# Optimization experiments

Hardware: AMD Instinct MI355X
Metric: run time of the kernel (lower is better)

## Reference

```python
import jax, jax.numpy as jnp
import numpy as np

N = 8192      # nodes
E = 16384     # edges
G = 512       # graphs
IN = 235      # node feature dim (input_dim)
H = 64        # hidden_dim
ED = 52       # edge feature dim


def setup_inputs() -> dict:
    key = jax.random.key(0)
    ks = jax.random.split(key, 24)
    s = lambda fan_in: 1.0 / np.sqrt(fan_in)
    inp = {}
    inp["x"] = jax.random.normal(ks[0], (N, IN), dtype=jnp.float32)
    inp["edge_index"] = jax.random.randint(ks[1], (2, E), 0, N)
    inp["edge_attr"] = jax.random.uniform(ks[2], (E, ED), dtype=jnp.float32)
    inp["batch"] = jnp.sort(jax.random.randint(ks[3], (N,), 0, G))
    # EdgeModel (nn of nnconv1): Linear(52,128) -> Linear(128, 235*64)
    inp["W1"] = jax.random.normal(ks[4], (128, ED), dtype=jnp.float32) * s(ED)
    inp["b1"] = jnp.zeros((128,), jnp.float32)
    inp["W2"] = jax.random.normal(ks[5], (IN * H, 128), dtype=jnp.float32) * s(128)
    inp["b2"] = jnp.zeros((IN * H,), jnp.float32)
    # NNConv root weight and bias
    inp["root"] = jax.random.normal(ks[6], (IN, H), dtype=jnp.float32) * s(IN)
    inp["conv_b"] = jnp.zeros((H,), jnp.float32)
    # MLP head
    inp["fw1"] = jax.random.normal(ks[7], (128, H), dtype=jnp.float32) * s(H)
    inp["fb1"] = jnp.zeros((128,), jnp.float32)
    inp["fw2"] = jax.random.normal(ks[8], (256, 128), dtype=jnp.float32) * s(128)
    inp["fb2"] = jnp.zeros((256,), jnp.float32)
    inp["fw3"] = jax.random.normal(ks[9], (128, 256), dtype=jnp.float32) * s(256)
    inp["fb3"] = jnp.zeros((128,), jnp.float32)
    inp["fw4"] = jax.random.normal(ks[10], (1, 128), dtype=jnp.float32) * s(128)
    inp["fb4"] = jnp.zeros((1,), jnp.float32)
    return inp


def reference(x, edge_index, edge_attr, batch, W1, b1, W2, b2, root, conv_b,
              fw1, fb1, fw2, fb2, fw3, fb3, fw4, fb4):
    src, dst = edge_index[0], edge_index[1]
    # edge MLP -> per-edge weight matrices [E, IN, H]
    h = edge_attr @ W1.T + b1
    w = (h @ W2.T + b2).reshape(E, IN, H)
    # gather source node feats, per-edge matmul, scatter-add to destinations
    msg = jnp.einsum('ei,eih->eh', x[src], w)          # [E, H]
    agg = jax.ops.segment_sum(msg, dst, num_segments=N)  # [N, H]
    out = jax.nn.relu(agg + x @ root + conv_b)           # NNConv + ReLU
    # global mean pool per graph
    summ = jax.ops.segment_sum(out, batch, num_segments=G)
    cnt = jax.ops.segment_sum(jnp.ones((N, 1), out.dtype), batch, num_segments=G)
    pooled = summ / jnp.maximum(cnt, 1.0)                # [G, H]
    # dense MLP head
    y = jax.nn.relu(pooled @ fw1.T + fb1)
    y = jax.nn.relu(y @ fw2.T + fb2)
    y = jax.nn.relu(y @ fw3.T + fb3)
    return y @ fw4.T + fb4                               # [G, 1]
```

## Files before the change

### kernel.cpp

```cpp
#include <hip/hip_runtime.h>
#include <hip/hip_bf16.h>
#include <stdint.h>

#define N_NODES 8192
#define N_EDGES 16384
#define N_GRAPHS 512
#define IN_DIM 235
#define H_DIM 64
#define ED_DIM 52
#define HID1 128
#define KP 256
#define NB 3328
#define NBE 3456

typedef __bf16 bf16x8 __attribute__((ext_vector_type(8)));
typedef float f32x4 __attribute__((ext_vector_type(4)));

static __device__ inline unsigned short f2bf(float f) {
    union { float f; unsigned u; } v; v.f = f;
    unsigned r = v.u + 0x7FFFu + ((v.u >> 16) & 1u);
    return (unsigned short)(r >> 16);
}
static __device__ inline float bf2f(unsigned short s) {
    union { unsigned u; float f; } v; v.u = ((unsigned)s) << 16;
    return v.f;
}

__global__ __launch_bounds__(256) void k_build_bt(const float* __restrict__ W1,
                                                  const float* __restrict__ W2,
                                                  unsigned short* __restrict__ Bt) {
    __shared__ float w1s[13 * HID1];
    __shared__ float w2s[64 * 132];
    const int i = blockIdx.x;
    const int by = blockIdx.y;
    const int t = threadIdx.x;
    const int dbase = by * 13;
    for (int j = t; j < 13 * HID1; j += 256) {
        const int dd = j >> 7, k = j & 127;
        w1s[j] = W1[k * ED_DIM + dbase + dd];
    }
    const float* w2src = W2 + (size_t)i * 64 * HID1;
    for (int j = t; j < 64 * HID1; j += 256) w2s[(j >> 7) * 132 + (j & 127)] = w2src[j];
    __syncthreads();
    const int pend = by * 832 + 832;
    for (int p = by * 832 + t; p < pend; p += 256) {
        const int dd = (p >> 6) - dbase, h = p & 63;
        const float4* w1v = (const float4*)&w1s[dd * HID1];
        const float4* w2v = (const float4*)&w2s[h * 132];
        float acc = 0.f;
        #pragma unroll
        for (int k4 = 0; k4 < HID1 / 4; ++k4) {
            const float4 a = w1v[k4], b = w2v[k4];
            acc += a.x * b.x + a.y * b.y + a.z * b.z + a.w * b.w;
        }
        Bt[(size_t)p * KP + i] = f2bf(acc);
    }
}

__global__ __launch_bounds__(256) void k_build_bc(const float* __restrict__ W2,
                                                  const float* __restrict__ b1,
                                                  const float* __restrict__ b2,
                                                  float* __restrict__ bc) {
    const int j = blockIdx.x * 256 + threadIdx.x;
    if (j >= IN_DIM * H_DIM) return;
    float acc = b2[j];
    const float* w = W2 + (size_t)j * HID1;
    #pragma unroll 8
    for (int k = 0; k < HID1; ++k) acc += w[k] * b1[k];
    bc[j] = acc;
}

__global__ __launch_bounds__(256) void k_build_ext(const float* __restrict__ root,
                                                   const float* __restrict__ bc,
                                                   unsigned short* __restrict__ Bt) {
    const int j = blockIdx.x;
    const int i = threadIdx.x;
    if (i >= IN_DIM) return;
    const float v = (j < 64) ? root[i * H_DIM + j] : bc[i * H_DIM + (j - 64)];
    Bt[(size_t)(NB + j) * KP + i] = f2bf(v);
}

__global__ __launch_bounds__(256) void k_build_a(const float* __restrict__ x,
                                                 unsigned short* __restrict__ A) {
    const int j = blockIdx.x * 256 + threadIdx.x;
    const int n = j >> 8, i = j & 255;
    A[j] = (i < IN_DIM) ? f2bf(x[n * IN_DIM + i]) : (unsigned short)0;
}

__global__ __launch_bounds__(256) void k_gemm(const unsigned short* __restrict__ A,
                                              const unsigned short* __restrict__ Bt,
                                              unsigned short* __restrict__ P,
                                              float* __restrict__ agg,
                                              float* __restrict__ xb2,
                                              const float* __restrict__ conv_b) {
    __shared__ unsigned short As[2 * 128 * 32];
    __shared__ unsigned short Bs[2 * 128 * 32];
    const int t = threadIdx.x;
    const int m0 = blockIdx.y * 128, n0 = blockIdx.x * 128;
    const int wid = t >> 6, lane = t & 63;
    const int wm = wid >> 1, wn = wid & 1;
    const int q = lane >> 4, r16 = lane & 15;

    f32x4 acc[4][4] = {};

    auto stage = [&](int k0, int buf) {
        #pragma unroll
        for (int r = 0; r < 2; ++r) {
            const int idx = r * 256 + t;
            const int row = idx >> 2;
            const int lgrp = ((idx & 3) ^ ((row >> 1) & 3)) * 8;
            const unsigned short* ga = &A[(size_t)(m0 + row) * KP + k0 + lgrp];
            const unsigned short* gb = &Bt[(size_t)(n0 + row) * KP + k0 + lgrp];
            char* la = (char*)As + buf * 8192 + r * 4096 + wid * 1024;
            char* lb = (char*)Bs + buf * 8192 + r * 4096 + wid * 1024;
            __builtin_amdgcn_global_load_lds(
                (const __attribute__((address_space(1))) unsigned int*)ga,
                (__attribute__((address_space(3))) unsigned int*)la, 16, 0, 0);
            __builtin_amdgcn_global_load_lds(
                (const __attribute__((address_space(1))) unsigned int*)gb,
                (__attribute__((address_space(3))) unsigned int*)lb, 16, 0, 0);
        }
    };

    stage(0, 0);
    const int pcq = (q ^ ((r16 >> 1) & 3)) * 8;
    #pragma unroll
    for (int it = 0; it < 8; ++it) {
        __syncthreads();
        if (it < 7) stage((it + 1) * 32, (it + 1) & 1);
        const int bo = (it & 1) * 4096;
        bf16x8 af[4], bfr[4];
        #pragma unroll
        for (int mi = 0; mi < 4; ++mi)
            af[mi] = *(const bf16x8*)(&As[bo + (wm * 64 + mi * 16 + r16) * 32 + pcq]);
        #pragma unroll
        for (int ni = 0; ni < 4; ++ni)
            bfr[ni] = *(const bf16x8*)(&Bs[bo + (wn * 64 + ni * 16 + r16) * 32 + pcq]);
        #pragma unroll
        for (int mi = 0; mi < 4; ++mi)
            #pragma unroll
            for (int ni = 0; ni < 4; ++ni)
                acc[mi][ni] = __builtin_amdgcn_mfma_f32_16x16x32_bf16(
                    bfr[ni], af[mi], acc[mi][ni], 0, 0, 0);
    }

    if (n0 < NB) {
        #pragma unroll
        for (int mi = 0; mi < 4; ++mi)
            #pragma unroll
            for (int ni = 0; ni < 4; ++ni) {
                const int row = m0 + wm * 64 + mi * 16 + r16;
                const int col = n0 + wn * 64 + ni * 16 + q * 4;
                union { unsigned short us[4]; uint2 u2; } pk;
                #pragma unroll
                for (int rr = 0; rr < 4; ++rr) pk.us[rr] = f2bf(acc[mi][ni][rr]);
                *(uint2*)(&P[(size_t)row * NB + col]) = pk.u2;
            }
    } else {
        #pragma unroll
        for (int mi = 0; mi < 4; ++mi)
            #pragma unroll
            for (int ni = 0; ni < 4; ++ni) {
                const int row = m0 + wm * 64 + mi * 16 + r16;
                const int cl = ni * 16 + q * 4;
                if (wn == 0) {
                    const float4 cb = *(const float4*)&conv_b[cl];
                    float4 v;
                    v.x = acc[mi][ni][0] + cb.x; v.y = acc[mi][ni][1] + cb.y;
                    v.z = acc[mi][ni][2] + cb.z; v.w = acc[mi][ni][3] + cb.w;
                    *(float4*)(&agg[row * H_DIM + cl]) = v;
                } else {
                    float4 v;
                    v.x = acc[mi][ni][0]; v.y = acc[mi][ni][1];
                    v.z = acc[mi][ni][2]; v.w = acc[mi][ni][3];
                    *(float4*)(&xb2[row * H_DIM + cl]) = v;
                }
            }
    }
}

__global__ __launch_bounds__(256) void k_edge(const int* __restrict__ ei,
                                              const float* __restrict__ ea,
                                              const unsigned short* __restrict__ P,
                                              const float* __restrict__ xb2,
                                              float* __restrict__ agg) {
    const int e = (blockIdx.x * 256 + threadIdx.x) >> 6;
    const int h = threadIdx.x & 63;
    if (e >= N_EDGES) return;
    const int s = ei[e], dst = ei[N_EDGES + e];
    const unsigned short* Pr = P + (size_t)s * NB + h;
    const float* ear = ea + (size_t)e * ED_DIM;

    float eav[ED_DIM];
    #pragma unroll
    for (int d4 = 0; d4 < ED_DIM / 4; ++d4)
        *(float4*)&eav[d4 * 4] = *(const float4*)&ear[d4 * 4];

    unsigned short pv[ED_DIM];
    #pragma unroll
    for (int d = 0; d < ED_DIM; ++d) pv[d] = Pr[d * H_DIM];

    float acc = xb2[s * H_DIM + h];
    #pragma unroll
    for (int d = 0; d < ED_DIM; ++d) acc += eav[d] * bf2f(pv[d]);
    atomicAdd(&agg[dst * H_DIM + h], acc);
}

__global__ __launch_bounds__(256) void k_pool(const float* __restrict__ agg,
                                              const int* __restrict__ batch,
                                              float* __restrict__ psum,
                                              float* __restrict__ pcnt) {
    const int n = (blockIdx.x * 256 + threadIdx.x) >> 6;
    const int h = threadIdx.x & 63;
    if (n >= N_NODES) return;
    const float v = fmaxf(agg[n * H_DIM + h], 0.f);
    const int g = batch[n];
    atomicAdd(&psum[g * H_DIM + h], v);
    if (h == 0) atomicAdd(&pcnt[g], 1.0f);
}

__global__ __launch_bounds__(256) void k_head(const float* __restrict__ psum,
                                              const float* __restrict__ pcnt,
                                              const float* __restrict__ fw1, const float* __restrict__ fb1,
                                              const float* __restrict__ fw2, const float* __restrict__ fb2,
                                              const float* __restrict__ fw3, const float* __restrict__ fb3,
                                              const float* __restrict__ fw4, const float* __restrict__ fb4,
                                              float* __restrict__ out) {
    __shared__ float sp[64], s1[128], s2[256], s3[128];
    const int g = blockIdx.x, t = threadIdx.x;
    if (t < 64) sp[t] = psum[g * 64 + t] / fmaxf(pcnt[g], 1.0f);
    __syncthreads();
    if (t < 128) {
        float a = fb1[t];
        const float* w = fw1 + t * 64;
        #pragma unroll 8
        for (int k = 0; k < 64; ++k) a += sp[k] * w[k];
        s1[t] = fmaxf(a, 0.f);
    }
    __syncthreads();
    {
        float a = fb2[t];
        const float* w = fw2 + t * 128;
        #pragma unroll 8
        for (int k = 0; k < 128; ++k) a += s1[k] * w[k];
        s2[t] = fmaxf(a, 0.f);
    }
    __syncthreads();
    if (t < 128) {
        float a = fb3[t];
        const float* w = fw3 + t * 256;
        #pragma unroll 8
        for (int k = 0; k < 256; ++k) a += s2[k] * w[k];
        s3[t] = fmaxf(a, 0.f);
    }
    __syncthreads();
    if (t < 64) {
        float p = s3[t] * fw4[t] + s3[t + 64] * fw4[t + 64];
        #pragma unroll
        for (int off = 32; off > 0; off >>= 1) p += __shfl_down(p, off);
        if (t == 0) out[g] = p + fb4[0];
    }
}

extern "C" void kernel_launch(void* const* d_in, const int* in_sizes, int n_in,
                              void* d_out, int out_size, void* d_ws, size_t ws_size,
                              hipStream_t stream) {
    const float* x      = (const float*)d_in[0];
    const int*   ei     = (const int*)d_in[1];
    const float* ea     = (const float*)d_in[2];
    const int*   batch  = (const int*)d_in[3];
    const float* W1     = (const float*)d_in[4];
    const float* b1     = (const float*)d_in[5];
    const float* W2     = (const float*)d_in[6];
    const float* b2     = (const float*)d_in[7];
    const float* root   = (const float*)d_in[8];
    const float* conv_b = (const float*)d_in[9];
    const float* fw1 = (const float*)d_in[10]; const float* fb1 = (const float*)d_in[11];
    const float* fw2 = (const float*)d_in[12]; const float* fb2 = (const float*)d_in[13];
    const float* fw3 = (const float*)d_in[14]; const float* fb3 = (const float*)d_in[15];
    const float* fw4 = (const float*)d_in[16]; const float* fb4 = (const float*)d_in[17];
    float* out = (float*)d_out;

    char* ws = (char*)d_ws;
    unsigned short* A   = (unsigned short*)(ws);
    unsigned short* Bt  = (unsigned short*)(ws + 4194304);
    unsigned short* P   = (unsigned short*)(ws + 5963776);
    float* agg  = (float*)(ws + 60489728);
    float* xb2  = (float*)(ws + 62586880);
    float* bc   = (float*)(ws + 64684032);
    float* psum = (float*)(ws + 64744192);
    float* pcnt = (float*)(ws + 64875264);

    hipMemsetAsync(Bt, 0, (size_t)NBE * KP * sizeof(unsigned short), stream);
    hipMemsetAsync(psum, 0, (size_t)(N_GRAPHS * H_DIM + N_GRAPHS) * sizeof(float), stream);

    k_build_bc<<<dim3((IN_DIM * H_DIM + 255) / 256), dim3(256), 0, stream>>>(W2, b1, b2, bc);
    k_build_bt<<<dim3(IN_DIM, 4), dim3(256), 0, stream>>>(W1, W2, Bt);
    k_build_ext<<<dim3(128), dim3(256), 0, stream>>>(root, bc, Bt);
    k_build_a<<<dim3(N_NODES), dim3(256), 0, stream>>>(x, A);
    k_gemm<<<dim3(NBE / 128, N_NODES / 128), dim3(256), 0, stream>>>(A, Bt, P, agg, xb2, conv_b);
    k_edge<<<dim3(N_EDGES / 4), dim3(256), 0, stream>>>(ei, ea, P, xb2, agg);
    k_pool<<<dim3(N_NODES / 4), dim3(256), 0, stream>>>(agg, batch, psum, pcnt);
    k_head<<<dim3(N_GRAPHS), dim3(256), 0, stream>>>(psum, pcnt, fw1, fb1, fw2, fb2, fw3, fb3, fw4, fb4, out);
}
```

Measured before the change: 228.8 us.

## Enlarge GEMM tile to 256x256 with 8 waves and fuse bias build into ext

The GEMM goes from 128x128 tiles with 4 waves to 256x256 tiles with 8 waves. Each wave now computes 128x64 (8x4 MFMA tiles), so every loaded fragment is reused more and the kernel does less global-to-LDS traffic. The B matrix is padded from 3456 to 3584 rows to fit the larger tile, and the extra padded columns are skipped in the epilogue. The separate bias-combination kernel is folded into k_build_ext, removing one launch. The cost is more accumulator registers, fewer blocks on the grid, and some wasted work on the padded columns.

```diff
diff --git a/kernel.cpp b/kernel.cpp
--- a/kernel.cpp
+++ b/kernel.cpp
@@ -12,6 +12,7 @@
 #define KP 256
 #define NB 3328
 #define NBE 3456
+#define NBP 3584
 
 typedef __bf16 bf16x8 __attribute__((ext_vector_type(8)));
 typedef float f32x4 __attribute__((ext_vector_type(4)));
@@ -57,26 +58,25 @@
     }
 }
 
-__global__ __launch_bounds__(256) void k_build_bc(const float* __restrict__ W2,
-                                                  const float* __restrict__ b1,
-                                                  const float* __restrict__ b2,
-                                                  float* __restrict__ bc) {
-    const int j = blockIdx.x * 256 + threadIdx.x;
-    if (j >= IN_DIM * H_DIM) return;
-    float acc = b2[j];
-    const float* w = W2 + (size_t)j * HID1;
-    #pragma unroll 8
-    for (int k = 0; k < HID1; ++k) acc += w[k] * b1[k];
-    bc[j] = acc;
-}
-
 __global__ __launch_bounds__(256) void k_build_ext(const float* __restrict__ root,
-                                                   const float* __restrict__ bc,
+                                                   const float* __restrict__ W2,
+                                                   const float* __restrict__ b1,
+                                                   const float* __restrict__ b2,
                                                    unsigned short* __restrict__ Bt) {
     const int j = blockIdx.x;
     const int i = threadIdx.x;
     if (i >= IN_DIM) return;
-    const float v = (j < 64) ? root[i * H_DIM + j] : bc[i * H_DIM + (j - 64)];
+    float v;
+    if (j < 64) {
+        v = root[i * H_DIM + j];
+    } else {
+        const int jj = i * H_DIM + (j - 64);
+        float acc = b2[jj];
+        const float* w = W2 + (size_t)jj * HID1;
+        #pragma unroll 8
+        for (int k = 0; k < HID1; ++k) acc += w[k] * b1[k];
+        v = acc;
+    }
     Bt[(size_t)(NB + j) * KP + i] = f2bf(v);
 }
 
@@ -87,32 +87,33 @@
     A[j] = (i < IN_DIM) ? f2bf(x[n * IN_DIM + i]) : (unsigned short)0;
 }
 
-__global__ __launch_bounds__(256) void k_gemm(const unsigned short* __restrict__ A,
-                                              const unsigned short* __restrict__ Bt,
-                                              unsigned short* __restrict__ P,
-                                              float* __restrict__ agg,
-                                              float* __restrict__ xb2,
-                                              const float* __restrict__ conv_b) {
-    __shared__ unsigned short As[2 * 128 * 32];
-    __shared__ unsigned short Bs[2 * 128 * 32];
+__global__ __launch_bounds__(512, 2) void k_gemm(const unsigned short* __restrict__ A,
+                                                 const unsigned short* __restrict__ Bt,
+                                                 unsigned short* __restrict__ P,
+                                                 float* __restrict__ agg,
+                                                 float* __restrict__ xb2,
+                                                 const float* __restrict__ conv_b) {
+    __shared__ unsigned short As[2 * 256 * 32];
+    __shared__ unsigned short Bs[2 * 256 * 32];
     const int t = threadIdx.x;
-    const int m0 = blockIdx.y * 128, n0 = blockIdx.x * 128;
+    const int m0 = blockIdx.y * 256, n0 = blockIdx.x * 256;
     const int wid = t >> 6, lane = t & 63;
-    const int wm = wid >> 1, wn = wid & 1;
+    const int wm = wid & 1;
+    const int wn = wid >> 1;
     const int q = lane >> 4, r16 = lane & 15;
 
-    f32x4 acc[4][4] = {};
+    f32x4 acc[8][4] = {};
 
     auto stage = [&](int k0, int buf) {
         #pragma unroll
         for (int r = 0; r < 2; ++r) {
-            const int idx = r * 256 + t;
+            const int idx = r * 512 + t;
             const int row = idx >> 2;
             const int lgrp = ((idx & 3) ^ ((row >> 1) & 3)) * 8;
             const unsigned short* ga = &A[(size_t)(m0 + row) * KP + k0 + lgrp];
             const unsigned short* gb = &Bt[(size_t)(n0 + row) * KP + k0 + lgrp];
-            char* la = (char*)As + buf * 8192 + r * 4096 + wid * 1024;
-            char* lb = (char*)Bs + buf * 8192 + r * 4096 + wid * 1024;
+            char* la = (char*)As + buf * 16384 + r * 8192 + wid * 1024;
+            char* lb = (char*)Bs + buf * 16384 + r * 8192 + wid * 1024;
             __builtin_amdgcn_global_load_lds(
                 (const __attribute__((address_space(1))) unsigned int*)ga,
                 (__attribute__((address_space(3))) unsigned int*)la, 16, 0, 0);
@@ -128,16 +129,16 @@
     for (int it = 0; it < 8; ++it) {
         __syncthreads();
         if (it < 7) stage((it + 1) * 32, (it + 1) & 1);
-        const int bo = (it & 1) * 4096;
-        bf16x8 af[4], bfr[4];
-        #pragma unroll
-        for (int mi = 0; mi < 4; ++mi)
-            af[mi] = *(const bf16x8*)(&As[bo + (wm * 64 + mi * 16 + r16) * 32 + pcq]);
+        const int bo = (it & 1) * 8192;
+        bf16x8 af[8], bfr[4];
+        #pragma unroll
+        for (int mi = 0; mi < 8; ++mi)
+            af[mi] = *(const bf16x8*)(&As[bo + (wm * 128 + mi * 16 + r16) * 32 + pcq]);
         #pragma unroll
         for (int ni = 0; ni < 4; ++ni)
             bfr[ni] = *(const bf16x8*)(&Bs[bo + (wn * 64 + ni * 16 + r16) * 32 + pcq]);
         #pragma unroll
-        for (int mi = 0; mi < 4; ++mi)
+        for (int mi = 0; mi < 8; ++mi)
             #pragma unroll
             for (int ni = 0; ni < 4; ++ni)
                 acc[mi][ni] = __builtin_amdgcn_mfma_f32_16x16x32_bf16(
@@ -146,22 +147,22 @@
 
     if (n0 < NB) {
         #pragma unroll
-        for (int mi = 0; mi < 4; ++mi)
+        for (int mi = 0; mi < 8; ++mi)
             #pragma unroll
             for (int ni = 0; ni < 4; ++ni) {
-                const int row = m0 + wm * 64 + mi * 16 + r16;
+                const int row = m0 + wm * 128 + mi * 16 + r16;
                 const int col = n0 + wn * 64 + ni * 16 + q * 4;
                 union { unsigned short us[4]; uint2 u2; } pk;
                 #pragma unroll
                 for (int rr = 0; rr < 4; ++rr) pk.us[rr] = f2bf(acc[mi][ni][rr]);
                 *(uint2*)(&P[(size_t)row * NB + col]) = pk.u2;
             }
-    } else {
-        #pragma unroll
-        for (int mi = 0; mi < 4; ++mi)
+    } else if (wn < 2) {
+        #pragma unroll
+        for (int mi = 0; mi < 8; ++mi)
             #pragma unroll
             for (int ni = 0; ni < 4; ++ni) {
-                const int row = m0 + wm * 64 + mi * 16 + r16;
+                const int row = m0 + wm * 128 + mi * 16 + r16;
                 const int cl = ni * 16 + q * 4;
                 if (wn == 0) {
                     const float4 cb = *(const float4*)&conv_b[cl];
@@ -284,21 +285,19 @@
     char* ws = (char*)d_ws;
     unsigned short* A   = (unsigned short*)(ws);
     unsigned short* Bt  = (unsigned short*)(ws + 4194304);
-    unsigned short* P   = (unsigned short*)(ws + 5963776);
-    float* agg  = (float*)(ws + 60489728);
-    float* xb2  = (float*)(ws + 62586880);
-    float* bc   = (float*)(ws + 64684032);
-    float* psum = (float*)(ws + 64744192);
-    float* pcnt = (float*)(ws + 64875264);
-
-    hipMemsetAsync(Bt, 0, (size_t)NBE * KP * sizeof(unsigned short), stream);
+    unsigned short* P   = (unsigned short*)(ws + 6029312);
+    float* agg  = (float*)(ws + 60555264);
+    float* xb2  = (float*)(ws + 62652416);
+    float* psum = (float*)(ws + 64749568);
+    float* pcnt = (float*)(ws + 64880640);
+
+    hipMemsetAsync(Bt, 0, (size_t)NBP * KP * sizeof(unsigned short), stream);
     hipMemsetAsync(psum, 0, (size_t)(N_GRAPHS * H_DIM + N_GRAPHS) * sizeof(float), stream);
 
-    k_build_bc<<<dim3((IN_DIM * H_DIM + 255) / 256), dim3(256), 0, stream>>>(W2, b1, b2, bc);
     k_build_bt<<<dim3(IN_DIM, 4), dim3(256), 0, stream>>>(W1, W2, Bt);
-    k_build_ext<<<dim3(128), dim3(256), 0, stream>>>(root, bc, Bt);
+    k_build_ext<<<dim3(128), dim3(256), 0, stream>>>(root, W2, b1, b2, Bt);
     k_build_a<<<dim3(N_NODES), dim3(256), 0, stream>>>(x, A);
-    k_gemm<<<dim3(NBE / 128, N_NODES / 128), dim3(256), 0, stream>>>(A, Bt, P, agg, xb2, conv_b);
+    k_gemm<<<dim3(NBP / 256, N_NODES / 256), dim3(512), 0, stream>>>(A, Bt, P, agg, xb2, conv_b);
     k_edge<<<dim3(N_EDGES / 4), dim3(256), 0, stream>>>(ei, ea, P, xb2, agg);
     k_pool<<<dim3(N_NODES / 4), dim3(256), 0, stream>>>(agg, batch, psum, pcnt);
     k_head<<<dim3(N_GRAPHS), dim3(256), 0, stream>>>(psum, pcnt, fw1, fb1, fw2, fb2, fw3, fb3, fw4, fb4, out);
```

Result: faster. 218.1 us (-4.7%).
